# Kernel optimization log

Hardware: AMD Instinct MI355X
Metric: run time of the kernel (lower is better)

## Reference

```python
import jax, jax.numpy as jnp
import numpy as np

B, N, C, F, E, K = 2, 2048, 1024, 4096, 8, 2

def setup_inputs() -> dict:
    key = jax.random.key(0)
    k = jax.random.split(key, 6)
    xavier1 = float(np.sqrt(6.0 / (C + F)))
    xavier2 = float(np.sqrt(6.0 / (F + C)))
    return {
        "x": jax.random.normal(k[0], (B, N, C), dtype=jnp.float32),
        "router_w": jax.random.normal(k[1], (E, C), dtype=jnp.float32) * 0.01,
        "w1": jax.random.uniform(k[2], (E, F, C), dtype=jnp.float32, minval=-xavier1, maxval=xavier1),
        "b1": jnp.zeros((E, F), dtype=jnp.float32),
        "w2": jax.random.uniform(k[3], (E, C, F), dtype=jnp.float32, minval=-xavier2, maxval=xavier2),
        "b2": jnp.zeros((E, C), dtype=jnp.float32),
    }

def reference(x, router_w, w1, b1, w2, b2):
    Bb, Nn, Cc = x.shape
    x_flat = x.reshape(-1, Cc)                                   # [T, C]
    # Router (eval mode: no noise)
    logits = jnp.einsum('tc,ec->te', x_flat, router_w)           # [T, E]
    probs = jax.nn.softmax(logits, axis=-1)
    top_w, top_idx = jax.lax.top_k(probs, K)                     # [T, K]
    top_w = top_w / (jnp.sum(top_w, axis=-1, keepdims=True) + 1e-9)
    # Dense all-expert MLP (same math as the per-expert gather/scatter loop)
    h = jnp.einsum('tc,efc->tef', x_flat, w1) + b1[None]          # [T, E, F]
    h = jax.nn.relu(h)
    y = jnp.einsum('tef,ecf->tec', h, w2) + b2[None]              # [T, E, C]
    # Gather the K selected experts per token and combine
    sel = jnp.take_along_axis(y, top_idx[:, :, None], axis=1)    # [T, K, C]
    out = jnp.einsum('tkc,tk->tc', sel, top_w)                   # [T, C]
    return out.reshape(Bb, Nn, Cc)
```

## Files before the change

### kernel.cpp

```cpp
#include <hip/hip_runtime.h>
#include <hip/hip_fp16.h>


#define T_TOK 4096
#define C_DIM 1024
#define F_DIM 4096
#define E_NUM 8
#define BM 128
#define BN 256
#define BK 64
#define MAXT 72
#define NP   (MAXT * BM)
#define TILE_H 8192

typedef float f32x4 __attribute__((ext_vector_type(4)));
typedef _Float16 half8 __attribute__((ext_vector_type(8)));

#define AS1 __attribute__((address_space(1)))
#define AS3 __attribute__((address_space(3)))

__device__ __forceinline__ int swz(int r, int ec) { return ec ^ ((r & 7) << 3); }

__device__ __forceinline__ half8 cvt8(float4 f0, float4 f1) {
  half8 hv;
  hv[0] = (_Float16)f0.x; hv[1] = (_Float16)f0.y; hv[2] = (_Float16)f0.z; hv[3] = (_Float16)f0.w;
  hv[4] = (_Float16)f1.x; hv[5] = (_Float16)f1.y; hv[6] = (_Float16)f1.z; hv[7] = (_Float16)f1.w;
  return hv;
}

__device__ __forceinline__ int xcd_swz(int bid, int nwg) {
  int xcd = bid & 7, rest = bid >> 3;
  int q = nwg >> 3, r = nwg & 7;
  return (xcd < r ? xcd * (q + 1) : r * (q + 1) + (xcd - r) * q) + rest;
}

__global__ __launch_bounds__(256) void router_kernel(
    const float* __restrict__ x, const float* __restrict__ rw,
    int* __restrict__ top_idx, float* __restrict__ top_w)
{
  int t = blockIdx.x * 4 + (threadIdx.x >> 6);
  int lane = threadIdx.x & 63;
  const float* xr = x + (size_t)t * C_DIM;
  float acc[E_NUM];
#pragma unroll
  for (int e = 0; e < E_NUM; ++e) acc[e] = 0.f;
  for (int j = 0; j < C_DIM / 64; ++j) {
    int c = j * 64 + lane;
    float xv = xr[c];
#pragma unroll
    for (int e = 0; e < E_NUM; ++e) acc[e] += xv * rw[e * C_DIM + c];
  }
#pragma unroll
  for (int e = 0; e < E_NUM; ++e) {
    float v = acc[e];
#pragma unroll
    for (int off = 32; off > 0; off >>= 1) v += __shfl_xor(v, off);
    acc[e] = v;
  }
  if (lane == 0) {
    float mx = acc[0];
    for (int e = 1; e < E_NUM; ++e) mx = fmaxf(mx, acc[e]);
    float p[E_NUM]; float Z = 0.f;
    for (int e = 0; e < E_NUM; ++e) { p[e] = expf(acc[e] - mx); Z += p[e]; }
    int b0 = 0;
    for (int e = 1; e < E_NUM; ++e) if (p[e] > p[b0]) b0 = e;
    int b1i = -1; float pb = -1.f;
    for (int e = 0; e < E_NUM; ++e) if (e != b0 && p[e] > pb) { pb = p[e]; b1i = e; }
    float p0 = p[b0] / Z, p1 = pb / Z;
    float s = p0 + p1 + 1e-9f;
    top_idx[t * 2 + 0] = b0;
    top_idx[t * 2 + 1] = b1i;
    top_w[t * 2 + 0] = p0 / s;
    top_w[t * 2 + 1] = p1 / s;
  }
}

__global__ void build_lists(const int* __restrict__ top_idx,
                            int* __restrict__ rows_g, int* __restrict__ counts,
                            int* __restrict__ tile_off, int* __restrict__ inv)
{
  int e = threadIdx.x >> 6;
  int lane = threadIdx.x & 63;
  int cnt = 0;
  for (int t0 = 0; t0 < T_TOK; t0 += 64) {
    int t = t0 + lane;
    bool sel = (top_idx[t * 2] == e) || (top_idx[t * 2 + 1] == e);
    cnt += __popcll(__ballot(sel));
  }
  if (lane == 0) counts[e] = cnt;
  __syncthreads();
  if (threadIdx.x == 0) {
    int o = 0;
    for (int i = 0; i < E_NUM; ++i) { tile_off[i] = o; o += (counts[i] + BM - 1) / BM; }
    tile_off[E_NUM] = o;
  }
  __syncthreads();
  int base = tile_off[e] * BM;
  int pos = 0;
  for (int t0 = 0; t0 < T_TOK; t0 += 64) {
    int t = t0 + lane;
    int i0 = top_idx[t * 2], i1 = top_idx[t * 2 + 1];
    bool sel = (i0 == e) || (i1 == e);
    unsigned long long mask = __ballot(sel);
    if (sel) {
      int p = pos + __popcll(mask & ((1ull << lane) - 1ull));
      int slot = t * 2 + ((i0 == e) ? 0 : 1);
      rows_g[base + p] = slot;
      inv[slot] = (e << 16) | (base + p);
    }
    pos += __popcll(mask);
  }
}

__global__ __launch_bounds__(256) void gather_x(
    const float* __restrict__ x, const int* __restrict__ rows_g,
    const int* __restrict__ counts, const int* __restrict__ tile_off,
    _Float16* __restrict__ xg)
{
  unsigned g = blockIdx.x * 256 + threadIdx.x;
  unsigned p = g >> 7, ccr = g & 127;
  int gt = p >> 7, r = p & 127;
  int kc = ccr >> 3, c8 = ccr & 7;
  int e = -1;
#pragma unroll
  for (int i = 0; i < E_NUM; ++i)
    if (gt >= tile_off[i] && gt < tile_off[i + 1]) e = i;
  half8 hv = {};
  if (e >= 0) {
    int nrem = counts[e] - (gt - tile_off[e]) * BM;
    if (r < nrem) {
      int t = rows_g[p] >> 1;
      const float4* s = reinterpret_cast<const float4*>(x + (size_t)t * C_DIM + kc * 64 + c8 * 8);
      hv = cvt8(s[0], s[1]);
    }
  }
  *reinterpret_cast<half8*>(xg + ((size_t)gt * 16 + kc) * TILE_H + r * 64 + ((c8 ^ (r & 7)) << 3)) = hv;
}

__global__ __launch_bounds__(256) void cvt_w1(
    const float* __restrict__ src, _Float16* __restrict__ dst, int ch, int Fc, int lgFc)
{
  unsigned g = blockIdx.x * 256 + threadIdx.x;
  unsigned row = g >> 7, ccr = g & 127;
  int e = row >> lgFc, frow = row & (Fc - 1);
  int ftl = frow >> 7, r = frow & 127;
  int kc = ccr >> 3, c8 = ccr & 7;
  const float4* s = reinterpret_cast<const float4*>(
      src + ((size_t)e * F_DIM + ch * Fc + frow) * C_DIM + kc * 64 + c8 * 8);
  int nft = Fc >> 7;
  size_t tix = ((size_t)(e * nft + ftl) * 16 + kc);
  *reinterpret_cast<half8*>(dst + tix * TILE_H + r * 64 + ((c8 ^ (r & 7)) << 3)) = cvt8(s[0], s[1]);
}

__global__ __launch_bounds__(256) void cvt_w2(
    const float* __restrict__ src, _Float16* __restrict__ dst, int ch, int Fc, int lgc)
{
  unsigned g = blockIdx.x * 256 + threadIdx.x;
  unsigned row = g >> lgc, ccr = g & ((Fc >> 3) - 1);
  int e = row >> 10, c = row & 1023;
  int ct = c >> 7, r = c & 127;
  int kc = ccr >> 3, c8 = ccr & 7;
  const float4* s = reinterpret_cast<const float4*>(
      src + (size_t)row * F_DIM + ch * Fc + kc * 64 + c8 * 8);
  int nkc = Fc >> 6;
  size_t tix = ((size_t)(e * 8 + ct) * nkc + kc);
  *reinterpret_cast<half8*>(dst + tix * TILE_H + r * 64 + ((c8 ^ (r & 7)) << 3)) = cvt8(s[0], s[1]);
}

#define STAGE_TILE(aSrc_, b0Src_, b1Src_)                                         \
  {                                                                               \
    _Pragma("unroll")                                                             \
    for (int i_ = 0; i_ < 2; ++i_) {                                              \
      int o_ = tid * 8 + i_ * 4096;                                               \
      __builtin_amdgcn_global_load_lds((const AS1 void*)((aSrc_) + o_),           \
          (AS3 void*)(&As[o_]), 16, 0, 0);                                        \
      __builtin_amdgcn_global_load_lds((const AS1 void*)((b0Src_) + o_),          \
          (AS3 void*)(&Bs[o_]), 16, 0, 0);                                        \
      __builtin_amdgcn_global_load_lds((const AS1 void*)((b1Src_) + o_),          \
          (AS3 void*)(&Bs[8192 + o_]), 16, 0, 0);                                 \
    }                                                                             \
  }

#define COMPUTE_TILE()                                                            \
  _Pragma("unroll")                                                               \
  for (int kk = 0; kk < BK; kk += 32) {                                           \
    const int klo = kk + (lane >> 4) * 8;                                         \
    half8 aF[4], bF[4];                                                           \
    _Pragma("unroll")                                                             \
    for (int m = 0; m < 4; ++m) {                                                 \
      int r = wr * 64 + m * 16 + (lane & 15);                                     \
      aF[m] = *reinterpret_cast<const half8*>(&As[r * BK + swz(r, klo)]);         \
    }                                                                             \
    _Pragma("unroll")                                                             \
    for (int n = 0; n < 4; ++n) {                                                 \
      int br = wc * 64 + n * 16 + (lane & 15);                                    \
      bF[n] = *reinterpret_cast<const half8*>(                                    \
          &Bs[(br >> 7) * 8192 + (br & 127) * 64 + swz(br, klo)]);                \
    }                                                                             \
    _Pragma("unroll")                                                             \
    for (int m = 0; m < 4; ++m)                                                   \
      _Pragma("unroll")                                                           \
      for (int n = 0; n < 4; ++n)                                                 \
        acc[m][n] = __builtin_amdgcn_mfma_f32_16x16x32_f16(aF[m], bF[n], acc[m][n], 0, 0, 0); \
  }

__global__ __launch_bounds__(512) void gemm1_kernel(
    const _Float16* __restrict__ xg, const _Float16* __restrict__ w1t,
    const float* __restrict__ b1, const int* __restrict__ counts,
    const int* __restrict__ tile_off, _Float16* __restrict__ ht,
    int ch, int Fc)
{
  const int NFT = Fc / BN;
  const int wgid = xcd_swz(blockIdx.x, gridDim.x);
  const int grp = wgid / (8 * NFT);
  const int rem = wgid - grp * 8 * NFT;
  const int ft = rem >> 3;
  const int gt = grp * 8 + (rem & 7);
  if (gt >= tile_off[E_NUM]) return;
  int e = 0;
  while (gt >= tile_off[e + 1]) ++e;
  const int nrem = min(counts[e] - (gt - tile_off[e]) * BM, BM);
  const int nftl = Fc >> 7;
  const _Float16* At  = xg + (size_t)gt * 16 * TILE_H;
  const _Float16* Bt0 = w1t + (size_t)(e * nftl + 2 * ft) * 16 * TILE_H;
  const _Float16* Bt1 = w1t + (size_t)(e * nftl + 2 * ft + 1) * 16 * TILE_H;

  __shared__ __align__(16) _Float16 As[TILE_H];
  __shared__ __align__(16) _Float16 Bs[2 * TILE_H];

  const int tid = threadIdx.x;
  const int lane = tid & 63;
  const int wave = tid >> 6;
  const int wr = wave >> 2, wc = wave & 3;

  f32x4 acc[4][4];
#pragma unroll
  for (int m = 0; m < 4; ++m)
#pragma unroll
    for (int n = 0; n < 4; ++n) acc[m][n] = (f32x4){0.f, 0.f, 0.f, 0.f};

  for (int kc = 0; kc < 16; ++kc) {
    STAGE_TILE(At + (size_t)kc * TILE_H, Bt0 + (size_t)kc * TILE_H, Bt1 + (size_t)kc * TILE_H);
    __syncthreads();
    COMPUTE_TILE();
    __syncthreads();
  }

  const int nkcF = Fc >> 6;
#pragma unroll
  for (int m = 0; m < 4; ++m) {
#pragma unroll
    for (int j = 0; j < 4; ++j) {
      int iloc = wr * 64 + m * 16 + (lane >> 4) * 4 + j;
      if (iloc < nrem) {
#pragma unroll
        for (int n = 0; n < 4; ++n) {
          int fl = ft * BN + wc * 64 + n * 16 + (lane & 15);
          float v = acc[m][n][j] + b1[e * F_DIM + ch * Fc + fl];
          _Float16 h = (_Float16)fmaxf(v, 0.f);
          ht[((size_t)gt * nkcF + (fl >> 6)) * TILE_H + iloc * 64 +
             ((((fl >> 3) & 7) ^ (iloc & 7)) << 3) + (fl & 7)] = h;
        }
      }
    }
  }
}

__global__ __launch_bounds__(512) void gemm2_kernel(
    const _Float16* __restrict__ ht, const _Float16* __restrict__ w2t,
    const int* __restrict__ tile_off, _Float16* __restrict__ y,
    int Fc, int kspl, int accum)
{
  const int NCMB = 4 * kspl;
  const int wgid = xcd_swz(blockIdx.x, gridDim.x);
  const int grp = wgid / (8 * NCMB);
  const int rem = wgid - grp * 8 * NCMB;
  const int cmb = rem >> 3;
  const int gt = grp * 8 + (rem & 7);
  if (gt >= tile_off[E_NUM]) return;
  const int ct = cmb & 3;
  const int ks = cmb >> 2;
  int e = 0;
  while (gt >= tile_off[e + 1]) ++e;
  const int nkc = Fc >> 6;
  const int klen = nkc / kspl;
  const _Float16* At  = ht + ((size_t)gt * nkc + ks * klen) * TILE_H;
  const _Float16* Bt0 = w2t + ((size_t)(e * 8 + 2 * ct) * nkc + ks * klen) * TILE_H;
  const _Float16* Bt1 = w2t + ((size_t)(e * 8 + 2 * ct + 1) * nkc + ks * klen) * TILE_H;

  __shared__ __align__(16) _Float16 As[TILE_H];
  __shared__ __align__(16) _Float16 Bs[2 * TILE_H];

  const int tid = threadIdx.x;
  const int lane = tid & 63;
  const int wave = tid >> 6;
  const int wr = wave >> 2, wc = wave & 3;

  f32x4 acc[4][4];
#pragma unroll
  for (int m = 0; m < 4; ++m)
#pragma unroll
    for (int n = 0; n < 4; ++n) acc[m][n] = (f32x4){0.f, 0.f, 0.f, 0.f};

  for (int kc = 0; kc < klen; ++kc) {
    STAGE_TILE(At + (size_t)kc * TILE_H, Bt0 + (size_t)kc * TILE_H, Bt1 + (size_t)kc * TILE_H);
    __syncthreads();
    COMPUTE_TILE();
    __syncthreads();
  }

  _Float16* yk = y + ((size_t)(ks * MAXT + gt) * BM) * C_DIM;
#pragma unroll
  for (int m = 0; m < 4; ++m) {
#pragma unroll
    for (int j = 0; j < 4; ++j) {
      int iloc = wr * 64 + m * 16 + (lane >> 4) * 4 + j;
#pragma unroll
      for (int n = 0; n < 4; ++n) {
        int c = ct * BN + wc * 64 + n * 16 + (lane & 15);
        _Float16* p = yk + (size_t)iloc * C_DIM + c;
        float v = acc[m][n][j];
        if (accum) v += (float)*p;
        *p = (_Float16)v;
      }
    }
  }
}

__global__ __launch_bounds__(256) void combine_kernel(
    const _Float16* __restrict__ y, const int* __restrict__ inv,
    const float* __restrict__ top_w, const float* __restrict__ b2,
    float* __restrict__ out, int kspl)
{
  int g = blockIdx.x * 256 + threadIdx.x;
  int t = g >> 7, c8 = (g & 127) << 3;
  float o[8];
#pragma unroll
  for (int i = 0; i < 8; ++i) o[i] = 0.f;
#pragma unroll
  for (int k = 0; k < 2; ++k) {
    int iv = inv[t * 2 + k];
    int e = iv >> 16, pos = iv & 0xffff;
    float w = top_w[t * 2 + k];
    const float4* bb = reinterpret_cast<const float4*>(b2 + e * C_DIM + c8);
    float4 bv0 = bb[0], bv1 = bb[1];
    float s[8] = {bv0.x, bv0.y, bv0.z, bv0.w, bv1.x, bv1.y, bv1.z, bv1.w};
    for (int ks = 0; ks < kspl; ++ks) {
      half8 hv = *reinterpret_cast<const half8*>(
          y + ((size_t)(ks * MAXT * BM + pos)) * C_DIM + c8);
#pragma unroll
      for (int i = 0; i < 8; ++i) s[i] += (float)hv[i];
    }
#pragma unroll
    for (int i = 0; i < 8; ++i) o[i] += w * s[i];
  }
  float4* op = reinterpret_cast<float4*>(out + (size_t)t * C_DIM + c8);
  op[0] = (float4){o[0], o[1], o[2], o[3]};
  op[1] = (float4){o[4], o[5], o[6], o[7]};
}

extern "C" void kernel_launch(void* const* d_in, const int* in_sizes, int n_in,
                              void* d_out, int out_size, void* d_ws, size_t ws_size,
                              hipStream_t stream)
{
  const float* x  = (const float*)d_in[0];
  const float* rw = (const float*)d_in[1];
  const float* w1 = (const float*)d_in[2];
  const float* b1 = (const float*)d_in[3];
  const float* w2 = (const float*)d_in[4];
  const float* b2 = (const float*)d_in[5];
  float* out = (float*)d_out;

  char* ws = (char*)d_ws;
  size_t off = 0;
  auto carve = [&](size_t bytes) -> void* {
    void* p = ws + off;
    off += (bytes + 255) & ~(size_t)255;
    return p;
  };
  int*   top_idx  = (int*)carve((size_t)T_TOK * 2 * sizeof(int));
  float* top_w    = (float*)carve((size_t)T_TOK * 2 * sizeof(float));
  int*   counts   = (int*)carve(E_NUM * sizeof(int));
  int*   tile_off = (int*)carve((E_NUM + 1) * sizeof(int));
  int*   rows_g   = (int*)carve((size_t)NP * sizeof(int));
  int*   inv      = (int*)carve((size_t)T_TOK * 2 * sizeof(int));
  _Float16* xg    = (_Float16*)carve((size_t)MAXT * 16 * TILE_H * sizeof(_Float16));
  _Float16* y     = (_Float16*)carve((size_t)2 * NP * C_DIM * sizeof(_Float16));
  size_t fixed = off;

  int nchunk = 8;
  const int cands[4] = {1, 2, 4, 8};
  for (int ci = 0; ci < 4; ++ci) {
    int n = cands[ci];
    size_t fc = (size_t)(F_DIM / n);
    size_t w1b = ((size_t)E_NUM * fc * C_DIM * 2 + 255) & ~(size_t)255;
    size_t w2b = ((size_t)E_NUM * C_DIM * fc * 2 + 255) & ~(size_t)255;
    size_t htb = ((size_t)MAXT * (fc >> 6) * TILE_H * 2 + 255) & ~(size_t)255;
    if (fixed + w1b + w2b + htb <= ws_size) { nchunk = n; break; }
  }
  const int Fc = F_DIM / nchunk;
  int lgFc = 0; while ((1 << lgFc) < Fc) ++lgFc;
  _Float16* w1t = (_Float16*)carve((size_t)E_NUM * Fc * C_DIM * sizeof(_Float16));
  _Float16* w2t = (_Float16*)carve((size_t)E_NUM * C_DIM * Fc * sizeof(_Float16));
  _Float16* ht  = (_Float16*)carve((size_t)MAXT * (Fc >> 6) * TILE_H * sizeof(_Float16));

  const int kspl = (Fc >= 2048) ? 2 : 1;

  router_kernel<<<T_TOK / 4, 256, 0, stream>>>(x, rw, top_idx, top_w);
  build_lists<<<1, 512, 0, stream>>>(top_idx, rows_g, counts, tile_off, inv);
  gather_x<<<(MAXT * BM * 128) / 256, 256, 0, stream>>>(x, rows_g, counts, tile_off, xg);

  const int cvt_blocks = 4 * Fc;
  for (int ch = 0; ch < nchunk; ++ch) {
    cvt_w1<<<cvt_blocks, 256, 0, stream>>>(w1, w1t, ch, Fc, lgFc);
    cvt_w2<<<cvt_blocks, 256, 0, stream>>>(w2, w2t, ch, Fc, lgFc - 3);
    gemm1_kernel<<<MAXT * (Fc / BN), 512, 0, stream>>>(
        xg, w1t, b1, counts, tile_off, ht, ch, Fc);
    gemm2_kernel<<<MAXT * 4 * kspl, 512, 0, stream>>>(
        ht, w2t, tile_off, y, Fc, kspl, ch != 0);
  }
  combine_kernel<<<(T_TOK * 128) / 256, 256, 0, stream>>>(y, inv, top_w, b2, out, kspl);
}
```

Baseline: 355.2 us.

## Shrink gemm2 output tile to 128x128 and make weight conversion writes contiguous

gemm2 now uses 128x128 output tiles with 4 waves and a single B tile per k-step, which doubles the grid to raise occupancy and parallelism in the second GEMM. The cost is less reuse of the A tile, since each A tile is now loaded twice as often. The w1/w2 conversion kernels now index by destination position, so their fp16 stores are fully sequential and the pre-swizzle happens on the read side. This trades scattered writes for more strided reads of the fp32 weights.

```diff
diff --git a/kernel.cpp b/kernel.cpp
--- a/kernel.cpp
+++ b/kernel.cpp
@@ -138,33 +138,39 @@
 }
 
 __global__ __launch_bounds__(256) void cvt_w1(
-    const float* __restrict__ src, _Float16* __restrict__ dst, int ch, int Fc, int lgFc)
+    const float* __restrict__ src, _Float16* __restrict__ dst, int ch, int Fc, int lgnftl)
 {
   unsigned g = blockIdx.x * 256 + threadIdx.x;
-  unsigned row = g >> 7, ccr = g & 127;
-  int e = row >> lgFc, frow = row & (Fc - 1);
-  int ftl = frow >> 7, r = frow & 127;
-  int kc = ccr >> 3, c8 = ccr & 7;
+  unsigned tile = g >> 10;
+  unsigned kc = tile & 15;
+  unsigned et = tile >> 4;
+  unsigned ftl = et & ((1u << lgnftl) - 1);
+  unsigned e = et >> lgnftl;
+  unsigned r = (g >> 3) & 127;
+  unsigned sc = g & 7;
+  unsigned c8 = sc ^ (r & 7);
+  unsigned frow = ftl * 128 + r;
   const float4* s = reinterpret_cast<const float4*>(
       src + ((size_t)e * F_DIM + ch * Fc + frow) * C_DIM + kc * 64 + c8 * 8);
-  int nft = Fc >> 7;
-  size_t tix = ((size_t)(e * nft + ftl) * 16 + kc);
-  *reinterpret_cast<half8*>(dst + tix * TILE_H + r * 64 + ((c8 ^ (r & 7)) << 3)) = cvt8(s[0], s[1]);
+  *reinterpret_cast<half8*>(dst + (size_t)g * 8) = cvt8(s[0], s[1]);
 }
 
 __global__ __launch_bounds__(256) void cvt_w2(
-    const float* __restrict__ src, _Float16* __restrict__ dst, int ch, int Fc, int lgc)
+    const float* __restrict__ src, _Float16* __restrict__ dst, int ch, int Fc, int lgnkc)
 {
   unsigned g = blockIdx.x * 256 + threadIdx.x;
-  unsigned row = g >> lgc, ccr = g & ((Fc >> 3) - 1);
-  int e = row >> 10, c = row & 1023;
-  int ct = c >> 7, r = c & 127;
-  int kc = ccr >> 3, c8 = ccr & 7;
+  unsigned tile = g >> 10;
+  unsigned kc = tile & ((1u << lgnkc) - 1);
+  unsigned et = tile >> lgnkc;
+  unsigned ct = et & 7;
+  unsigned e = et >> 3;
+  unsigned r = (g >> 3) & 127;
+  unsigned sc = g & 7;
+  unsigned c8 = sc ^ (r & 7);
+  unsigned c = ct * 128 + r;
   const float4* s = reinterpret_cast<const float4*>(
-      src + (size_t)row * F_DIM + ch * Fc + kc * 64 + c8 * 8);
-  int nkc = Fc >> 6;
-  size_t tix = ((size_t)(e * 8 + ct) * nkc + kc);
-  *reinterpret_cast<half8*>(dst + tix * TILE_H + r * 64 + ((c8 ^ (r & 7)) << 3)) = cvt8(s[0], s[1]);
+      src + ((size_t)e * C_DIM + c) * F_DIM + ch * Fc + kc * 64 + c8 * 8);
+  *reinterpret_cast<half8*>(dst + (size_t)g * 8) = cvt8(s[0], s[1]);
 }
 
 #define STAGE_TILE(aSrc_, b0Src_, b1Src_)                                         \
@@ -196,6 +202,40 @@
       int br = wc * 64 + n * 16 + (lane & 15);                                    \
       bF[n] = *reinterpret_cast<const half8*>(                                    \
           &Bs[(br >> 7) * 8192 + (br & 127) * 64 + swz(br, klo)]);                \
+    }                                                                             \
+    _Pragma("unroll")                                                             \
+    for (int m = 0; m < 4; ++m)                                                   \
+      _Pragma("unroll")                                                           \
+      for (int n = 0; n < 4; ++n)                                                 \
+        acc[m][n] = __builtin_amdgcn_mfma_f32_16x16x32_f16(aF[m], bF[n], acc[m][n], 0, 0, 0); \
+  }
+
+#define STAGE2(aSrc_, bSrc_)                                                      \
+  {                                                                               \
+    _Pragma("unroll")                                                             \
+    for (int i_ = 0; i_ < 4; ++i_) {                                              \
+      int o_ = tid * 8 + i_ * 2048;                                               \
+      __builtin_amdgcn_global_load_lds((const AS1 void*)((aSrc_) + o_),           \
+          (AS3 void*)(&As[o_]), 16, 0, 0);                                        \
+      __builtin_amdgcn_global_load_lds((const AS1 void*)((bSrc_) + o_),           \
+          (AS3 void*)(&Bs[o_]), 16, 0, 0);                                        \
+    }                                                                             \
+  }
+
+#define COMPUTE2()                                                                \
+  _Pragma("unroll")                                                               \
+  for (int kk = 0; kk < BK; kk += 32) {                                           \
+    const int klo = kk + (lane >> 4) * 8;                                         \
+    half8 aF[4], bF[4];                                                           \
+    _Pragma("unroll")                                                             \
+    for (int m = 0; m < 4; ++m) {                                                 \
+      int r = wr * 64 + m * 16 + (lane & 15);                                     \
+      aF[m] = *reinterpret_cast<const half8*>(&As[r * BK + swz(r, klo)]);         \
+    }                                                                             \
+    _Pragma("unroll")                                                             \
+    for (int n = 0; n < 4; ++n) {                                                 \
+      int r = wc * 64 + n * 16 + (lane & 15);                                     \
+      bF[n] = *reinterpret_cast<const half8*>(&Bs[r * BK + swz(r, klo)]);         \
     }                                                                             \
     _Pragma("unroll")                                                             \
     for (int m = 0; m < 4; ++m)                                                   \
@@ -266,35 +306,34 @@
   }
 }
 
-__global__ __launch_bounds__(512) void gemm2_kernel(
+__global__ __launch_bounds__(256) void gemm2_kernel(
     const _Float16* __restrict__ ht, const _Float16* __restrict__ w2t,
     const int* __restrict__ tile_off, _Float16* __restrict__ y,
     int Fc, int kspl, int accum)
 {
-  const int NCMB = 4 * kspl;
+  const int NCMB = 8 * kspl;
   const int wgid = xcd_swz(blockIdx.x, gridDim.x);
   const int grp = wgid / (8 * NCMB);
   const int rem = wgid - grp * 8 * NCMB;
   const int cmb = rem >> 3;
   const int gt = grp * 8 + (rem & 7);
   if (gt >= tile_off[E_NUM]) return;
-  const int ct = cmb & 3;
-  const int ks = cmb >> 2;
+  const int ct = cmb & 7;
+  const int ks = cmb >> 3;
   int e = 0;
   while (gt >= tile_off[e + 1]) ++e;
   const int nkc = Fc >> 6;
   const int klen = nkc / kspl;
-  const _Float16* At  = ht + ((size_t)gt * nkc + ks * klen) * TILE_H;
-  const _Float16* Bt0 = w2t + ((size_t)(e * 8 + 2 * ct) * nkc + ks * klen) * TILE_H;
-  const _Float16* Bt1 = w2t + ((size_t)(e * 8 + 2 * ct + 1) * nkc + ks * klen) * TILE_H;
+  const _Float16* At = ht + ((size_t)gt * nkc + ks * klen) * TILE_H;
+  const _Float16* Bt = w2t + ((size_t)(e * 8 + ct) * nkc + ks * klen) * TILE_H;
 
   __shared__ __align__(16) _Float16 As[TILE_H];
-  __shared__ __align__(16) _Float16 Bs[2 * TILE_H];
+  __shared__ __align__(16) _Float16 Bs[TILE_H];
 
   const int tid = threadIdx.x;
   const int lane = tid & 63;
   const int wave = tid >> 6;
-  const int wr = wave >> 2, wc = wave & 3;
+  const int wr = wave >> 1, wc = wave & 1;
 
   f32x4 acc[4][4];
 #pragma unroll
@@ -303,9 +342,9 @@
     for (int n = 0; n < 4; ++n) acc[m][n] = (f32x4){0.f, 0.f, 0.f, 0.f};
 
   for (int kc = 0; kc < klen; ++kc) {
-    STAGE_TILE(At + (size_t)kc * TILE_H, Bt0 + (size_t)kc * TILE_H, Bt1 + (size_t)kc * TILE_H);
+    STAGE2(At + (size_t)kc * TILE_H, Bt + (size_t)kc * TILE_H);
     __syncthreads();
-    COMPUTE_TILE();
+    COMPUTE2();
     __syncthreads();
   }
 
@@ -317,7 +356,7 @@
       int iloc = wr * 64 + m * 16 + (lane >> 4) * 4 + j;
 #pragma unroll
       for (int n = 0; n < 4; ++n) {
-        int c = ct * BN + wc * 64 + n * 16 + (lane & 15);
+        int c = ct * 128 + wc * 64 + n * 16 + (lane & 15);
         _Float16* p = yk + (size_t)iloc * C_DIM + c;
         float v = acc[m][n][j];
         if (accum) v += (float)*p;
@@ -412,11 +451,11 @@
 
   const int cvt_blocks = 4 * Fc;
   for (int ch = 0; ch < nchunk; ++ch) {
-    cvt_w1<<<cvt_blocks, 256, 0, stream>>>(w1, w1t, ch, Fc, lgFc);
-    cvt_w2<<<cvt_blocks, 256, 0, stream>>>(w2, w2t, ch, Fc, lgFc - 3);
+    cvt_w1<<<cvt_blocks, 256, 0, stream>>>(w1, w1t, ch, Fc, lgFc - 7);
+    cvt_w2<<<cvt_blocks, 256, 0, stream>>>(w2, w2t, ch, Fc, lgFc - 6);
     gemm1_kernel<<<MAXT * (Fc / BN), 512, 0, stream>>>(
         xg, w1t, b1, counts, tile_off, ht, ch, Fc);
-    gemm2_kernel<<<MAXT * 4 * kspl, 512, 0, stream>>>(
+    gemm2_kernel<<<MAXT * 8 * kspl, 256, 0, stream>>>(
         ht, w2t, tile_off, y, Fc, kspl, ch != 0);
   }
   combine_kernel<<<(T_TOK * 128) / 256, 256, 0, stream>>>(y, inv, top_w, b2, out, kspl);
```

Result: no change. 355.5 us (+0.1%).
